# Kernel optimization log

Hardware: AMD Instinct MI355X
Metric: run time of the kernel (lower is better)

## Reference

```python
import jax, jax.numpy as jnp
import numpy as np

# Soft decision tree: heap-ordered full binary tree.
# Inner node n (0-based heap index) has gate p_n = sigmoid(beta_n * (x @ W_n + b_n)).
# Children of n are 2n+1 (left, prob 1-p) and 2n+2 (right, prob p).

LMBDA = 0.1


def setup_inputs() -> dict:
    key = jax.random.key(0)
    k = jax.random.split(key, 6)
    B, IN, OUT, D = 8192, 2048, 100, 8
    N = 2 ** D - 1          # inner nodes = 255
    L = 2 ** D              # leaves = 256
    x = jax.random.normal(k[0], (B, IN), dtype=jnp.float32)
    labels = jax.random.randint(k[1], (B,), 0, OUT, dtype=jnp.int32)
    W = jax.random.normal(k[2], (N, IN), dtype=jnp.float32) * 0.02
    b = jax.random.normal(k[3], (N,), dtype=jnp.float32) * 0.02
    beta = jax.random.normal(k[4], (N,), dtype=jnp.float32)
    leaf_params = jax.random.normal(k[5], (L, OUT), dtype=jnp.float32)
    return {"x": x, "labels": labels, "W": W, "b": b, "beta": beta,
            "leaf_params": leaf_params}


def _tree_paths(p, depth):
    """p: [B, N] gate probs in heap order. Returns (inner_path [B,N], leaf_path [B,L])."""
    B = p.shape[0]
    path = jnp.ones((B, 1), p.dtype)
    inner_paths = []
    start = 0
    for d in range(depth):
        width = 2 ** d
        p_lvl = p[:, start:start + width]          # [B, width]
        inner_paths.append(path)                   # path prob arriving at each inner node
        left = path * (1.0 - p_lvl)
        right = path * p_lvl
        # interleave -> heap order of next level: [l0, r0, l1, r1, ...]
        path = jnp.stack([left, right], axis=-1).reshape(B, 2 * width)
        start += width
    return jnp.concatenate(inner_paths, axis=1), path


def reference(x, labels, W, b, beta, leaf_params):
    N = W.shape[0]
    D = int(np.log2(N + 1))            # max_depth
    OUT = leaf_params.shape[1]

    # All inner-node gates in one GEMM: sigmoid(beta * (x @ W^T + b))
    p = jax.nn.sigmoid(beta[None, :] * (x @ W.T + b[None, :]))   # [B, N]
    inner_path, leaf_path = _tree_paths(p, D)                    # [B,N], [B,L]

    # Leaf distributions: softmax over each leaf's params
    logQ = jax.nn.log_softmax(leaf_params, axis=-1)              # [L, OUT]
    Q = jnp.exp(logQ)                                            # [L, OUT]

    # y one-hot; TQ[b, l] = y_b . log Q_l
    y = jax.nn.one_hot(labels, OUT, dtype=x.dtype)               # [B, OUT]
    TQ = y @ logQ.T                                              # [B, L]
    loss = jnp.mean(jnp.sum(leaf_path * TQ, axis=1))
    neg_loss = -loss

    # Penalty: only inner nodes whose children are also inner (depth 1..D-1)
    n_pen = 2 ** (D - 1) - 1
    alpha = jnp.sum(p * inner_path, axis=0) / jnp.sum(inner_path, axis=0)  # [N]
    node_idx = np.arange(N)
    depths = np.floor(np.log2(node_idx + 1)).astype(np.int32) + 1
    lmbda_arr = jnp.asarray(LMBDA * (2.0 ** (-depths)), dtype=x.dtype)     # [N]
    a = alpha[:n_pen]
    C = -jnp.sum(lmbda_arr[:n_pen] * 0.5 * (jnp.log(a) + jnp.log1p(-a)))

    # Output: leaf distribution of the max-path-prob leaf per sample
    best_leaf = jnp.argmax(leaf_path, axis=1)                    # [B]
    output = Q[best_leaf]                                        # [B, OUT]

    return neg_loss, output, C
```

## Files before the change

kernel.cpp:

```cpp
#include <hip/hip_runtime.h>
#include <math.h>

typedef __attribute__((ext_vector_type(4)))  short short4v;
typedef __attribute__((ext_vector_type(8)))  short short8v;
typedef __attribute__((ext_vector_type(4)))  float f32x4;

#define OFF_LOGQT 256
#define OFF_Q     25856
#define OFF_WHI   51456
#define OFF_WLO   313600
#define OFF_PART  575744
#define PART_STRIDE 2097152

__device__ __forceinline__ unsigned short f2bf(float f) {
    unsigned int b = __float_as_uint(f);
    unsigned int r = (b + 0x7FFFu + ((b >> 16) & 1u)) >> 16;
    return (unsigned short)r;
}
__device__ __forceinline__ float bf2f(unsigned short u) {
    return __uint_as_float(((unsigned int)u) << 16);
}
__device__ __forceinline__ void gl16(const void* g, void* l) {
    __builtin_amdgcn_global_load_lds(
        (const __attribute__((address_space(1))) unsigned int*)g,
        (__attribute__((address_space(3))) unsigned int*)l, 16, 0, 0);
}

__global__ __launch_bounds__(256) void k_prep(const float* __restrict__ W,
                                              unsigned short* __restrict__ whi,
                                              unsigned short* __restrict__ wlo,
                                              const float* __restrict__ lp,
                                              float* __restrict__ logQT,
                                              float* __restrict__ Q,
                                              float* __restrict__ accum)
{
    const int bx = blockIdx.x, tid = threadIdx.x;
    if (bx < 256) {
        if (bx == 0) accum[tid] = 0.f;
        int g = (bx * 256 + tid) * 8;
        int row = g >> 11;
        int c   = g & 2047;
        int sc  = c ^ ((row & 7) << 3);
        unsigned short h[8], l[8];
        if (row < 255) {
            const float* src = W + (size_t)row * 2048 + c;
            float4 v0 = *(const float4*)src;
            float4 v1 = *(const float4*)(src + 4);
            float vv[8] = {v0.x, v0.y, v0.z, v0.w, v1.x, v1.y, v1.z, v1.w};
#pragma unroll
            for (int j = 0; j < 8; ++j) {
                h[j] = f2bf(vv[j]);
                l[j] = f2bf(vv[j] - bf2f(h[j]));
            }
        } else {
#pragma unroll
            for (int j = 0; j < 8; ++j) { h[j] = 0; l[j] = 0; }
        }
        size_t dst = (size_t)row * 2048 + sc;
#pragma unroll
        for (int j = 0; j < 8; ++j) { whi[dst + j] = h[j]; wlo[dst + j] = l[j]; }
    } else {
        int w = tid >> 6, lane = tid & 63;
        int r = (bx - 256) * 4 + w;
        float v0 = (lane < 100)      ? lp[r * 100 + lane]      : -INFINITY;
        float v1 = (lane + 64 < 100) ? lp[r * 100 + lane + 64] : -INFINITY;
        float m = fmaxf(v0, v1);
        for (int s = 32; s; s >>= 1) m = fmaxf(m, __shfl_xor(m, s));
        float e = 0.f;
        if (lane < 100)      e += expf(v0 - m);
        if (lane + 64 < 100) e += expf(v1 - m);
        for (int s = 32; s; s >>= 1) e += __shfl_xor(e, s);
        float logZ = m + logf(e);
        if (lane < 100) {
            float lq = v0 - logZ;
            Q[r * 100 + lane] = expf(lq);
            logQT[lane * 256 + r] = lq;
        }
        if (lane + 64 < 100) {
            float lq = v1 - logZ;
            Q[r * 100 + lane + 64] = expf(lq);
            logQT[(lane + 64) * 256 + r] = lq;
        }
    }
}

__global__ __launch_bounds__(256, 2) void k_gemm3(const float* __restrict__ x,
                                                  const unsigned short* __restrict__ whi,
                                                  const unsigned short* __restrict__ wlo,
                                                  float* __restrict__ part,
                                                  int ksteps)
{
    __shared__ __align__(16) unsigned short Ah[64 * 64];
    __shared__ __align__(16) unsigned short Al[64 * 64];
    __shared__ __align__(16) unsigned short Bh[256 * 64];
    __shared__ __align__(16) unsigned short Bl[256 * 64];

    const int tid = threadIdx.x;
    const int w = tid >> 6, lane = tid & 63;
    const int r16 = lane & 15, hb = lane >> 4;
    const int row0 = blockIdx.x * 64;
    const int kz = blockIdx.z;
    float* pdst = part + (size_t)kz * PART_STRIDE;

    f32x4 acc[4][4] = {};
    float4 aR[4];

    for (int s = 0; s < ksteps; ++s) {
        const int k0 = (kz * ksteps + s) * 64;
#pragma unroll
        for (int it = 0; it < 4; ++it) {
            int ch = it * 256 + tid;
            int r = ch >> 4, c = (ch & 15) * 4;
            aR[it] = *(const float4*)(x + (size_t)(row0 + r) * 2048 + k0 + c);
        }
#pragma unroll
        for (int it = 0; it < 8; ++it) {
            int ch = it * 256 + tid;
            int r = ch >> 3, c = (ch & 7) * 8;
            gl16(whi + (size_t)r * 2048 + k0 + c, &Bh[ch * 8]);
            gl16(wlo + (size_t)r * 2048 + k0 + c, &Bl[ch * 8]);
        }
#pragma unroll
        for (int it = 0; it < 4; ++it) {
            int ch = it * 256 + tid;
            int r = ch >> 4, c = (ch & 15) * 4;
            int sc = c ^ ((r & 7) << 3);
            float vv[4] = {aR[it].x, aR[it].y, aR[it].z, aR[it].w};
            short4v hv, lv;
#pragma unroll
            for (int j = 0; j < 4; ++j) {
                unsigned short hbv = f2bf(vv[j]);
                hv[j] = (short)hbv;
                lv[j] = (short)f2bf(vv[j] - bf2f(hbv));
            }
            *(short4v*)&Ah[r * 64 + sc] = hv;
            *(short4v*)&Al[r * 64 + sc] = lv;
        }
        __syncthreads();
#pragma unroll
        for (int kk = 0; kk < 2; ++kk) {
            const int kc = kk * 32 + hb * 8;
            short8v ah[4], al[4];
#pragma unroll
            for (int fm = 0; fm < 4; ++fm) {
                int r = fm * 16 + r16;
                int idx = r * 64 + (kc ^ ((r & 7) << 3));
                ah[fm] = *(const short8v*)&Ah[idx];
                al[fm] = *(const short8v*)&Al[idx];
            }
#pragma unroll
            for (int fn = 0; fn < 4; ++fn) {
                int br = w * 64 + fn * 16 + r16;
                int bidx = br * 64 + (kc ^ ((br & 7) << 3));
                short8v bhh = *(const short8v*)&Bh[bidx];
                short8v bll = *(const short8v*)&Bl[bidx];
#pragma unroll
                for (int fm = 0; fm < 4; ++fm) {
                    acc[fm][fn] = __builtin_amdgcn_mfma_f32_16x16x32_bf16(ah[fm], bhh, acc[fm][fn], 0, 0, 0);
                    acc[fm][fn] = __builtin_amdgcn_mfma_f32_16x16x32_bf16(ah[fm], bll, acc[fm][fn], 0, 0, 0);
                    acc[fm][fn] = __builtin_amdgcn_mfma_f32_16x16x32_bf16(al[fm], bhh, acc[fm][fn], 0, 0, 0);
                }
            }
        }
        __syncthreads();
    }

#pragma unroll
    for (int fm = 0; fm < 4; ++fm)
#pragma unroll
        for (int fn = 0; fn < 4; ++fn) {
            int col = w * 64 + fn * 16 + r16;
#pragma unroll
            for (int j = 0; j < 4; ++j) {
                int row = row0 + fm * 16 + hb * 4 + j;
                pdst[(size_t)row * 256 + col] = acc[fm][fn][j];
            }
        }
}

__global__ __launch_bounds__(256) void k_tree(const float* __restrict__ part, int npart,
                                              const float* __restrict__ bias,
                                              const float* __restrict__ beta,
                                              const int* __restrict__ labels,
                                              const float* __restrict__ logQT,
                                              const float* __restrict__ Q,
                                              float* __restrict__ accum,
                                              float* __restrict__ out)
{
    __shared__ float psh[4][256];
    __shared__ float redPI[4][128];
    __shared__ float redI[4][128];
    __shared__ float lossw[4];
    const int tid = threadIdx.x;
    const int w = tid >> 6, lane = tid & 63;
    const int c0 = lane * 4;

    float4 bi, be;
    if (lane < 63) {
        bi = *(const float4*)&bias[c0];
        be = *(const float4*)&beta[c0];
    } else {
        bi = make_float4(bias[252], bias[253], bias[254], 0.f);
        be = make_float4(beta[252], beta[253], beta[254], 0.f);
    }

    float aPI0 = 0.f, aPI1 = 0.f, aI0 = 0.f, aI1 = 0.f, lossAcc = 0.f;

    for (int rr = 0; rr < 4; ++rr) {
        int b = blockIdx.x * 16 + w * 4 + rr;

        float4 s = make_float4(0.f, 0.f, 0.f, 0.f);
        for (int z = 0; z < npart; ++z) {
            float4 v = *(const float4*)&part[(size_t)z * PART_STRIDE + (size_t)b * 256 + c0];
            s.x += v.x; s.y += v.y; s.z += v.z; s.w += v.w;
        }
        float4 pv;
        pv.x = 1.f / (1.f + expf(-be.x * (s.x + bi.x)));
        pv.y = 1.f / (1.f + expf(-be.y * (s.y + bi.y)));
        pv.z = 1.f / (1.f + expf(-be.z * (s.z + bi.z)));
        pv.w = 1.f / (1.f + expf(-be.w * (s.w + bi.w)));
        *(float4*)&psh[w][c0] = pv;
        asm volatile("s_waitcnt lgkmcnt(0)" ::: "memory");
        __builtin_amdgcn_sched_barrier(0);

        int label = labels[b];
        float4 tq = *(const float4*)&logQT[(size_t)label * 256 + c0];

        float prefix = 1.f;
#pragma unroll
        for (int d = 0; d < 6; ++d) {
            int node = (1 << d) - 1 + (lane >> (6 - d));
            float g = psh[w][node];
            prefix *= ((lane >> (5 - d)) & 1) ? g : (1.f - g);
        }
        float g6  = psh[w][63 + lane];
        float p60 = prefix * (1.f - g6), p61 = prefix * g6;
        float g7a = psh[w][127 + 2 * lane];
        float g7b = psh[w][128 + 2 * lane];
        float f0 = p60 * (1.f - g7a), f1 = p60 * g7a;
        float f2 = p61 * (1.f - g7b), f3 = p61 * g7b;

        float lsum = f0 * tq.x + f1 * tq.y + f2 * tq.z + f3 * tq.w;

        float best = f0; int bestIdx = c0;
        if (f1 > best) { best = f1; bestIdx = c0 + 1; }
        if (f2 > best) { best = f2; bestIdx = c0 + 2; }
        if (f3 > best) { best = f3; bestIdx = c0 + 3; }

        for (int sft = 32; sft; sft >>= 1) lsum += __shfl_xor(lsum, sft);
        for (int sft = 32; sft; sft >>= 1) {
            float ov = __shfl_xor(best, sft);
            int   oi = __shfl_xor(bestIdx, sft);
            if (ov > best || (ov == best && oi < bestIdx)) { best = ov; bestIdx = oi; }
        }
        lossAcc += lsum;

        {
            int n = lane;
            float f = 1.f;
            int cur = n;
            while (cur > 0) {
                int par = (cur - 1) >> 1;
                float g = psh[w][par];
                f *= (cur == 2 * par + 2) ? g : (1.f - g);
                cur = par;
            }
            aPI0 += psh[w][n] * f;
            aI0  += f;
        }
        if (lane < 63) {
            int n = lane + 64;
            float f = 1.f;
            int cur = n;
            while (cur > 0) {
                int par = (cur - 1) >> 1;
                float g = psh[w][par];
                f *= (cur == 2 * par + 2) ? g : (1.f - g);
                cur = par;
            }
            aPI1 += psh[w][n] * f;
            aI1  += f;
        }

        const float* qrow = Q + (size_t)bestIdx * 100;
        float* orow = out + 1 + (size_t)b * 100;
        orow[lane] = qrow[lane];
        if (lane < 36) orow[64 + lane] = qrow[64 + lane];
    }

    redPI[w][lane] = aPI0;           redI[w][lane] = aI0;
    redPI[w][64 + lane] = (lane < 63) ? aPI1 : 0.f;
    redI [w][64 + lane] = (lane < 63) ? aI1  : 0.f;
    if (lane == 0) lossw[w] = lossAcc;
    __syncthreads();
    if (tid < 127) {
        float sPI = redPI[0][tid] + redPI[1][tid] + redPI[2][tid] + redPI[3][tid];
        float sI  = redI [0][tid] + redI [1][tid] + redI [2][tid] + redI [3][tid];
        atomicAdd(&accum[1 + tid],   sPI);
        atomicAdd(&accum[128 + tid], sI);
    }
    if (tid == 128) {
        atomicAdd(&accum[0], lossw[0] + lossw[1] + lossw[2] + lossw[3]);
    }
}

__global__ __launch_bounds__(128) void k_final(const float* __restrict__ accum,
                                               float* __restrict__ out)
{
    __shared__ float s[128];
    int t = threadIdx.x;
    float term = 0.f;
    if (t < 127) {
        float a = accum[1 + t] / accum[128 + t];
        int depth = 32 - __clz(t + 1);
        float lmbda = 0.1f * exp2f(-(float)depth);
        term = -lmbda * 0.5f * (logf(a) + log1pf(-a));
    }
    s[t] = term;
    __syncthreads();
    if (t == 0) {
        float c = 0.f;
        for (int i = 0; i < 127; ++i) c += s[i];
        out[819201] = c;
        out[0] = -accum[0] / 8192.0f;
    }
}

extern "C" void kernel_launch(void* const* d_in, const int* in_sizes, int n_in,
                              void* d_out, int out_size, void* d_ws, size_t ws_size,
                              hipStream_t stream)
{
    const float* x      = (const float*)d_in[0];
    const int*   labels = (const int*)  d_in[1];
    const float* W      = (const float*)d_in[2];
    const float* bias   = (const float*)d_in[3];
    const float* beta   = (const float*)d_in[4];
    const float* leaf   = (const float*)d_in[5];
    float* out = (float*)d_out;
    float* ws  = (float*)d_ws;

    float*          accum = ws;
    float*          logQT = ws + OFF_LOGQT;
    float*          Q     = ws + OFF_Q;
    unsigned short* whi   = (unsigned short*)(ws + OFF_WHI);
    unsigned short* wlo   = (unsigned short*)(ws + OFF_WLO);
    float*          part  = ws + OFF_PART;

    auto need = [](int k) { return (size_t)(OFF_PART + (size_t)k * PART_STRIDE) * sizeof(float); };
    int ksplit = (ws_size >= need(4)) ? 4 : (ws_size >= need(2)) ? 2 : 1;

    k_prep<<<320, 256, 0, stream>>>(W, whi, wlo, leaf, logQT, Q, accum);
    k_gemm3<<<dim3(128, 1, ksplit), 256, 0, stream>>>(x, whi, wlo, part, 32 / ksplit);
    k_tree<<<512, 256, 0, stream>>>(part, ksplit, bias, beta, labels, logQT, Q, accum, out);
    k_final<<<1, 128, 0, stream>>>(accum, out);
}
```

Baseline: 163.2 us.

## Double-buffer split-bf16 GEMM with packed hi/lo weights and 128x128 tiles

Packs the hi and lo bf16 halves of W into one interleaved, swizzled buffer so each 32-wide K block loads both halves as a single 64-element row. The GEMM switches to 128x128 output tiles over a 2D grid and double-buffers LDS, so the next stage's global loads and x conversion overlap the current stage's MFMAs and one barrier per step is dropped. The tree kernel processes half as many rows per block with twice the blocks. The cost is more LDS per block, which may limit occupancy, and a larger register footprint from the prefetch.

```diff
diff --git a/kernel.cpp b/kernel.cpp
--- a/kernel.cpp
+++ b/kernel.cpp
@@ -7,8 +7,7 @@
 
 #define OFF_LOGQT 256
 #define OFF_Q     25856
-#define OFF_WHI   51456
-#define OFF_WLO   313600
+#define OFF_WPK   51456
 #define OFF_PART  575744
 #define PART_STRIDE 2097152
 
@@ -27,8 +26,7 @@
 }
 
 __global__ __launch_bounds__(256) void k_prep(const float* __restrict__ W,
-                                              unsigned short* __restrict__ whi,
-                                              unsigned short* __restrict__ wlo,
+                                              unsigned short* __restrict__ wpk,
                                               const float* __restrict__ lp,
                                               float* __restrict__ logQT,
                                               float* __restrict__ Q,
@@ -38,12 +36,11 @@
     if (bx < 256) {
         if (bx == 0) accum[tid] = 0.f;
         int g = (bx * 256 + tid) * 8;
-        int row = g >> 11;
-        int c   = g & 2047;
-        int sc  = c ^ ((row & 7) << 3);
+        int n = g >> 11;
+        int c = g & 2047;
         unsigned short h[8], l[8];
-        if (row < 255) {
-            const float* src = W + (size_t)row * 2048 + c;
+        if (n < 255) {
+            const float* src = W + (size_t)n * 2048 + c;
             float4 v0 = *(const float4*)src;
             float4 v1 = *(const float4*)(src + 4);
             float vv[8] = {v0.x, v0.y, v0.z, v0.w, v1.x, v1.y, v1.z, v1.w};
@@ -56,9 +53,13 @@
 #pragma unroll
             for (int j = 0; j < 8; ++j) { h[j] = 0; l[j] = 0; }
         }
-        size_t dst = (size_t)row * 2048 + sc;
-#pragma unroll
-        for (int j = 0; j < 8; ++j) { whi[dst + j] = h[j]; wlo[dst + j] = l[j]; }
+        size_t db = (size_t)n * 4096 + (size_t)(c >> 5) * 64;
+        int lc = (c >> 3) & 3;
+        int sw = n & 7;
+        unsigned short* hd = wpk + db + (size_t)((lc ^ sw) << 3);
+        unsigned short* ld = wpk + db + (size_t)(((4 + lc) ^ sw) << 3);
+#pragma unroll
+        for (int j = 0; j < 8; ++j) { hd[j] = h[j]; ld[j] = l[j]; }
     } else {
         int w = tid >> 6, lane = tid & 63;
         int r = (bx - 256) * 4 + w;
@@ -84,95 +85,115 @@
     }
 }
 
-__global__ __launch_bounds__(256, 2) void k_gemm3(const float* __restrict__ x,
-                                                  const unsigned short* __restrict__ whi,
-                                                  const unsigned short* __restrict__ wlo,
+__global__ __launch_bounds__(256, 2) void k_gemm4(const float* __restrict__ x,
+                                                  const unsigned short* __restrict__ wpk,
                                                   float* __restrict__ part,
                                                   int ksteps)
 {
-    __shared__ __align__(16) unsigned short Ah[64 * 64];
-    __shared__ __align__(16) unsigned short Al[64 * 64];
-    __shared__ __align__(16) unsigned short Bh[256 * 64];
-    __shared__ __align__(16) unsigned short Bl[256 * 64];
+    __shared__ __align__(16) unsigned short At[2][128 * 64];
+    __shared__ __align__(16) unsigned short Bt[2][128 * 64];
 
     const int tid = threadIdx.x;
     const int w = tid >> 6, lane = tid & 63;
+    const int wm = w >> 1, wn = w & 1;
     const int r16 = lane & 15, hb = lane >> 4;
-    const int row0 = blockIdx.x * 64;
+    const int row0 = blockIdx.x * 128;
+    const int col0 = blockIdx.y * 128;
     const int kz = blockIdx.z;
+    const int kblk0 = kz * ksteps;
     float* pdst = part + (size_t)kz * PART_STRIDE;
 
+    const int ar_ = tid >> 1, ahalf = tid & 1;
+
     f32x4 acc[4][4] = {};
-    float4 aR[4];
-
-    for (int s = 0; s < ksteps; ++s) {
-        const int k0 = (kz * ksteps + s) * 64;
+
+    auto GLA = [&](int s, float4* a) {
+        const float* src = x + (size_t)(row0 + ar_) * 2048 + (kblk0 + s) * 32 + ahalf * 16;
+#pragma unroll
+        for (int it = 0; it < 4; ++it) a[it] = ((const float4*)src)[it];
+    };
+    auto GLB = [&](int s, int bi) {
+        const int kblk = kblk0 + s;
 #pragma unroll
         for (int it = 0; it < 4; ++it) {
             int ch = it * 256 + tid;
-            int r = ch >> 4, c = (ch & 15) * 4;
-            aR[it] = *(const float4*)(x + (size_t)(row0 + r) * 2048 + k0 + c);
-        }
-#pragma unroll
-        for (int it = 0; it < 8; ++it) {
-            int ch = it * 256 + tid;
-            int r = ch >> 3, c = (ch & 7) * 8;
-            gl16(whi + (size_t)r * 2048 + k0 + c, &Bh[ch * 8]);
-            gl16(wlo + (size_t)r * 2048 + k0 + c, &Bl[ch * 8]);
-        }
+            int r = ch >> 3, c = ch & 7;
+            gl16(wpk + (size_t)(col0 + r) * 4096 + kblk * 64 + c * 8, &Bt[bi][ch * 8]);
+        }
+    };
+    auto CONVA = [&](const float4* a, int bi) {
+        float vv[16];
 #pragma unroll
         for (int it = 0; it < 4; ++it) {
-            int ch = it * 256 + tid;
-            int r = ch >> 4, c = (ch & 15) * 4;
-            int sc = c ^ ((r & 7) << 3);
-            float vv[4] = {aR[it].x, aR[it].y, aR[it].z, aR[it].w};
-            short4v hv, lv;
+            vv[it * 4 + 0] = a[it].x; vv[it * 4 + 1] = a[it].y;
+            vv[it * 4 + 2] = a[it].z; vv[it * 4 + 3] = a[it].w;
+        }
+        unsigned short h[16], l[16];
+#pragma unroll
+        for (int j = 0; j < 16; ++j) {
+            h[j] = f2bf(vv[j]);
+            l[j] = f2bf(vv[j] - bf2f(h[j]));
+        }
+        const int base = ar_ * 64, sw = ar_ & 7;
+#pragma unroll
+        for (int q = 0; q < 2; ++q) {
+            int lcH = ahalf * 2 + q;
+            short8v hv, lv;
+#pragma unroll
+            for (int j = 0; j < 8; ++j) { hv[j] = (short)h[q * 8 + j]; lv[j] = (short)l[q * 8 + j]; }
+            *(short8v*)&At[bi][base + ((lcH ^ sw) << 3)]       = hv;
+            *(short8v*)&At[bi][base + (((4 + lcH) ^ sw) << 3)] = lv;
+        }
+    };
+    auto COMPUTE = [&](int bi) {
+        short8v ah[4], al[4];
+#pragma unroll
+        for (int fm = 0; fm < 4; ++fm) {
+            int ar = wm * 64 + fm * 16 + r16;
+            int ab = ar * 64, sw = ar & 7;
+            ah[fm] = *(const short8v*)&At[bi][ab + ((hb ^ sw) << 3)];
+            al[fm] = *(const short8v*)&At[bi][ab + (((4 + hb) ^ sw) << 3)];
+        }
+#pragma unroll
+        for (int fn = 0; fn < 4; ++fn) {
+            int br = wn * 64 + fn * 16 + r16;
+            int bb = br * 64, sw = br & 7;
+            short8v bhh = *(const short8v*)&Bt[bi][bb + ((hb ^ sw) << 3)];
+            short8v bll = *(const short8v*)&Bt[bi][bb + (((4 + hb) ^ sw) << 3)];
+#pragma unroll
+            for (int fm = 0; fm < 4; ++fm) {
+                acc[fm][fn] = __builtin_amdgcn_mfma_f32_16x16x32_bf16(ah[fm], bhh, acc[fm][fn], 0, 0, 0);
+                acc[fm][fn] = __builtin_amdgcn_mfma_f32_16x16x32_bf16(ah[fm], bll, acc[fm][fn], 0, 0, 0);
+                acc[fm][fn] = __builtin_amdgcn_mfma_f32_16x16x32_bf16(al[fm], bhh, acc[fm][fn], 0, 0, 0);
+            }
+        }
+    };
+
+    float4 a0[4];
+    GLA(0, a0);
+    GLB(0, 0);
+    CONVA(a0, 0);
+    __syncthreads();
+
+    int buf = 0;
+    for (int s = 0; s < ksteps; ++s) {
+        float4 aN[4];
+        const bool pre = (s + 1 < ksteps);
+        if (pre) { GLA(s + 1, aN); GLB(s + 1, buf ^ 1); }
+        COMPUTE(buf);
+        if (pre) CONVA(aN, buf ^ 1);
+        __syncthreads();
+        buf ^= 1;
+    }
+
+#pragma unroll
+    for (int fm = 0; fm < 4; ++fm)
+#pragma unroll
+        for (int fn = 0; fn < 4; ++fn) {
+            int col = col0 + wn * 64 + fn * 16 + r16;
 #pragma unroll
             for (int j = 0; j < 4; ++j) {
-                unsigned short hbv = f2bf(vv[j]);
-                hv[j] = (short)hbv;
-                lv[j] = (short)f2bf(vv[j] - bf2f(hbv));
-            }
-            *(short4v*)&Ah[r * 64 + sc] = hv;
-            *(short4v*)&Al[r * 64 + sc] = lv;
-        }
-        __syncthreads();
-#pragma unroll
-        for (int kk = 0; kk < 2; ++kk) {
-            const int kc = kk * 32 + hb * 8;
-            short8v ah[4], al[4];
-#pragma unroll
-            for (int fm = 0; fm < 4; ++fm) {
-                int r = fm * 16 + r16;
-                int idx = r * 64 + (kc ^ ((r & 7) << 3));
-                ah[fm] = *(const short8v*)&Ah[idx];
-                al[fm] = *(const short8v*)&Al[idx];
-            }
-#pragma unroll
-            for (int fn = 0; fn < 4; ++fn) {
-                int br = w * 64 + fn * 16 + r16;
-                int bidx = br * 64 + (kc ^ ((br & 7) << 3));
-                short8v bhh = *(const short8v*)&Bh[bidx];
-                short8v bll = *(const short8v*)&Bl[bidx];
-#pragma unroll
-                for (int fm = 0; fm < 4; ++fm) {
-                    acc[fm][fn] = __builtin_amdgcn_mfma_f32_16x16x32_bf16(ah[fm], bhh, acc[fm][fn], 0, 0, 0);
-                    acc[fm][fn] = __builtin_amdgcn_mfma_f32_16x16x32_bf16(ah[fm], bll, acc[fm][fn], 0, 0, 0);
-                    acc[fm][fn] = __builtin_amdgcn_mfma_f32_16x16x32_bf16(al[fm], bhh, acc[fm][fn], 0, 0, 0);
-                }
-            }
-        }
-        __syncthreads();
-    }
-
-#pragma unroll
-    for (int fm = 0; fm < 4; ++fm)
-#pragma unroll
-        for (int fn = 0; fn < 4; ++fn) {
-            int col = w * 64 + fn * 16 + r16;
-#pragma unroll
-            for (int j = 0; j < 4; ++j) {
-                int row = row0 + fm * 16 + hb * 4 + j;
+                int row = row0 + wm * 64 + fm * 16 + hb * 4 + j;
                 pdst[(size_t)row * 256 + col] = acc[fm][fn][j];
             }
         }
@@ -206,8 +227,8 @@
 
     float aPI0 = 0.f, aPI1 = 0.f, aI0 = 0.f, aI1 = 0.f, lossAcc = 0.f;
 
-    for (int rr = 0; rr < 4; ++rr) {
-        int b = blockIdx.x * 16 + w * 4 + rr;
+    for (int rr = 0; rr < 2; ++rr) {
+        int b = blockIdx.x * 8 + w * 2 + rr;
 
         float4 s = make_float4(0.f, 0.f, 0.f, 0.f);
         for (int z = 0; z < npart; ++z) {
@@ -342,15 +363,15 @@
     float*          accum = ws;
     float*          logQT = ws + OFF_LOGQT;
     float*          Q     = ws + OFF_Q;
-    unsigned short* whi   = (unsigned short*)(ws + OFF_WHI);
-    unsigned short* wlo   = (unsigned short*)(ws + OFF_WLO);
+    unsigned short* wpk   = (unsigned short*)(ws + OFF_WPK);
     float*          part  = ws + OFF_PART;
 
     auto need = [](int k) { return (size_t)(OFF_PART + (size_t)k * PART_STRIDE) * sizeof(float); };
     int ksplit = (ws_size >= need(4)) ? 4 : (ws_size >= need(2)) ? 2 : 1;
-
-    k_prep<<<320, 256, 0, stream>>>(W, whi, wlo, leaf, logQT, Q, accum);
-    k_gemm3<<<dim3(128, 1, ksplit), 256, 0, stream>>>(x, whi, wlo, part, 32 / ksplit);
-    k_tree<<<512, 256, 0, stream>>>(part, ksplit, bias, beta, labels, logQT, Q, accum, out);
+    int ksteps = 64 / ksplit;
+
+    k_prep<<<320, 256, 0, stream>>>(W, wpk, leaf, logQT, Q, accum);
+    k_gemm4<<<dim3(64, 2, ksplit), 256, 0, stream>>>(x, wpk, part, ksteps);
+    k_tree<<<1024, 256, 0, stream>>>(part, ksplit, bias, beta, labels, logQT, Q, accum, out);
     k_final<<<1, 128, 0, stream>>>(accum, out);
 }
```

Result: slower. 182.3 us (+11.7%).
